# Kernel optimization log

Measured on AMD Instinct MI355X. Metric: run time of the kernel, lower is better.

## Reference

```python
import jax, jax.numpy as jnp
import numpy as np

B, TXT_T, MEL_T, N_MEL = 32, 256, 1600, 40
PAD_MAG = 1.0e12


def setup_inputs() -> dict:
    key = jax.random.key(0)
    k1, k2, k3, k4 = jax.random.split(key, 4)
    mu_logvar = jax.random.normal(k1, (B, TXT_T, 2 * N_MEL), jnp.float32)
    z = jax.random.normal(k2, (B, N_MEL, MEL_T), jnp.float32)
    text_lengths = jax.random.randint(k3, (B,), TXT_T // 2, TXT_T + 1).astype(jnp.int32)
    mel_lengths = jax.random.randint(k4, (B,), MEL_T // 2, MEL_T + 1).astype(jnp.int32)
    return {"mu_logvar": mu_logvar, "z": z,
            "text_lengths": text_lengths, "mel_lengths": mel_lengths}


def _mdn_log_prob(mu_logvar, z):
    # mu_logvar: [B, L, 2C], z: [B, C, T] -> log_prob_matrix [B, L, T]
    C = z.shape[1]
    mu, logvar = jnp.split(mu_logvar, 2, axis=-1)          # [B, L, C] each
    invvar = jnp.exp(-logvar)                               # [B, L, C]
    # mean_c((z - mu)^2 * invvar) expanded via matmuls (no [B,L,T,C] tensor)
    t1 = jnp.einsum('bct,blc->blt', z * z, invvar)
    t2 = jnp.einsum('bct,blc->blt', z, mu * invvar)
    t3 = jnp.sum(mu * mu * invvar, axis=-1)[:, :, None]
    mse = t1 - 2.0 * t2 + t3                                # [B, L, T]
    return -0.5 * (mse / C + jnp.mean(logvar, axis=-1)[:, :, None])


def _forward_dp(lp):
    # forward algorithm: log_alpha over (txt position, mel time) via scan over T
    Bb, L, T = lp.shape
    alpha0 = jnp.full((Bb, L + 1), -PAD_MAG, lp.dtype).at[:, 1].set(lp[:, 0, 0])

    def step(alpha, lp_t):
        stay = alpha[:, 1:] + 1e-7
        go = alpha[:, :-1] + 1e-7
        new = jnp.logaddexp(stay, go) + lp_t                # [B, L]
        alpha_new = jnp.concatenate(
            [jnp.full((Bb, 1), -PAD_MAG, lp.dtype), new], axis=1)
        return alpha_new, new

    _, ys = jax.lax.scan(step, alpha0, jnp.moveaxis(lp[:, :, 1:], 2, 0))
    log_alpha = jnp.concatenate([alpha0[:, 1:][None], ys], axis=0)  # [T, B, L]
    return log_alpha


def _viterbi(lp, text_lengths, mel_lengths):
    Bb, L, T = lp.shape
    beta0 = jnp.full((Bb, L), -PAD_MAG, lp.dtype).at[:, 0].set(lp[:, 0, 0])

    def fstep(beta, lp_t):
        shifted = jnp.concatenate(
            [jnp.full((Bb, 1), -PAD_MAG, lp.dtype), beta[:, :-1]], axis=1)
        new = jnp.maximum(beta, shifted) + lp_t
        return new, new

    _, ys = jax.lax.scan(fstep, beta0, jnp.moveaxis(lp[:, :, 1:], 2, 0))
    log_beta = jnp.transpose(jnp.concatenate([beta0[None], ys], axis=0), (1, 2, 0))  # [B, L, T]

    b_idx = jnp.arange(Bb)
    r0 = (text_lengths - 1).astype(jnp.float32)
    c0 = (mel_lengths - 1).astype(jnp.float32)

    def bstep(carry, _):
        rows, cols = carry
        ri = rows.astype(jnp.int32)
        ci = cols.astype(jnp.int32)
        # torch negative indexing wraps -> emulate with mod
        val_go = log_beta[b_idx, (ri - 1) % L, (ci - 1) % T]
        val_stay = log_beta[b_idx, ri % L, (ci - 1) % T]
        is_go = (val_go > val_stay).astype(rows.dtype)
        new_rows = jax.nn.relu(rows - is_go + 1.0) - 1.0
        new_cols = jax.nn.relu(cols) - 1.0
        return (new_rows, new_cols), new_rows

    _, path_ys = jax.lax.scan(bstep, (r0, c0), None, length=T - 1)
    full = jnp.concatenate([r0[None], path_ys], axis=0)     # [T, B], backward order
    path = full[::-1].T                                     # [B, T], chronological
    align = jax.nn.one_hot(path.astype(jnp.int32), L, dtype=lp.dtype)  # [B, T, L]

    def shift(a, ml):
        # F.pad(..., (-pad, pad)) on time axis: shift valid region to the front
        rolled = jnp.roll(a, -(T - ml), axis=0)
        mask = (jnp.arange(T) < ml)[:, None].astype(a.dtype)
        return rolled * mask

    return jax.vmap(shift)(align, mel_lengths)              # [B, T, L]


def reference(mu_logvar, z, text_lengths, mel_lengths):
    lp = _mdn_log_prob(mu_logvar, z)                        # [B, L, T]
    log_alpha = _forward_dp(lp)                             # [T, B, L]
    b_idx = jnp.arange(lp.shape[0])
    alpha_last = log_alpha[mel_lengths - 1, b_idx, text_lengths - 1]
    mdn_loss = -(alpha_last / mel_lengths.astype(alpha_last.dtype))  # [B]
    alignment = _viterbi(lp, text_lengths, mel_lengths)     # [B, T, L]
    return mdn_loss, alignment, lp
```

## Files before the change

### kernel.cpp

```cpp
#include <hip/hip_runtime.h>
#include <cstdint>
#include <math.h>

#define BB   32
#define LLEN 256
#define TLEN 1600
#define NC   40
#define NEGPADF (-1.0e12f)
#define NEGPADD (-1.0e12)
#define NBATCH 8
#define NPROD  4
#define NBUF   2

#define OFF_ALIGN 32
#define OFF_LP    (32 + (size_t)BB * TLEN * LLEN)

#define WSB_A    0
#define WSB_KC   (WSB_A + (size_t)BB * LLEN * 80 * 8)
#define WSB_LPT  (WSB_KC + (size_t)BB * LLEN * 8)
#define WSB_PATH (WSB_LPT + (size_t)BB * TLEN * LLEN * 4)

__device__ __forceinline__ int imin(int a, int b) { return a < b ? a : b; }

#define WAIT_LGKM0 0xC07F

__device__ __forceinline__ void bar_prod() {
  asm volatile("" ::: "memory");
  __builtin_amdgcn_s_waitcnt(WAIT_LGKM0);
  __builtin_amdgcn_s_barrier();
  asm volatile("" ::: "memory");
}
__device__ __forceinline__ void bar_cons() {
  asm volatile("" ::: "memory");
  __builtin_amdgcn_s_barrier();
  asm volatile("" ::: "memory");
}

__device__ __forceinline__ int rot1_i32(int x) {
  return __builtin_amdgcn_mov_dpp(x, 0x13C , 0xF, 0xF, true);
}
__device__ __forceinline__ float rot1_f32(float x) {
  return __int_as_float(rot1_i32(__float_as_int(x)));
}
__device__ __forceinline__ double rot1_f64(double x) {
  long long v = __double_as_longlong(x);
  int lo = rot1_i32((int)(v & 0xffffffffLL));
  int hi = rot1_i32((int)(v >> 32));
  return __longlong_as_double(((long long)hi << 32) | (unsigned long long)(unsigned int)lo);
}

__global__ __launch_bounds__(256) void prep_kernel(
    const float* __restrict__ mu_logvar, double* __restrict__ A, double* __restrict__ Kc) {
  int row = blockIdx.x * 4 + (threadIdx.x >> 6);
  int lane = threadIdx.x & 63;
  const float* src = mu_logvar + (size_t)row * (2 * NC);
  double mu = 0.0, lv = 0.0, iv = 0.0, part = 0.0;
  if (lane < NC) {
    mu = (double)src[lane];
    lv = (double)src[NC + lane];
    iv = exp(-lv);
    part = mu * mu * iv + lv;
  }
  for (int m = 1; m < 64; m <<= 1) part += __shfl_xor(part, m, 64);
  const double s = -0.5 / (double)NC;
  if (lane < NC) {
    A[(size_t)row * 80 + lane]      = s * iv;
    A[(size_t)row * 80 + NC + lane] = (1.0 / (double)NC) * mu * iv;
  }
  if (lane == 0) Kc[row] = s * part;
}

__global__ __launch_bounds__(128) void lp_kernel(
    const float* __restrict__ z, const double* __restrict__ A,
    const double* __restrict__ Kc, float* __restrict__ out,
    float* __restrict__ lpTh) {
  int b  = blockIdx.z;
  int l0 = blockIdx.y * 32;
  int t0 = blockIdx.x * 128;
  int tid = threadIdx.x;
  int t = t0 + tid;
  int tv = imin(t, TLEN - 1);
  bool act = (t < TLEN);

  float* lp_out = out + OFF_LP;
  float* loS    = out + OFF_ALIGN;

  float zr[NC];
  const float* zb = z + (size_t)b * NC * TLEN;
  #pragma unroll
  for (int c = 0; c < NC; ++c) zr[c] = zb[(size_t)c * TLEN + tv];

  __shared__ __align__(16) double tile[128][17];
  const double* Ab = A + ((size_t)b * LLEN + l0) * 80;
  const double* Kb = Kc + (size_t)b * LLEN + l0;

  for (int g = 0; g < 2; ++g) {
    for (int j16 = 0; j16 < 16; ++j16) {
      int j = g * 16 + j16;
      const double* Ar = Ab + (size_t)j * 80;
      double a0 = Kb[j], a1 = 0.0, a2 = 0.0, a3 = 0.0;
      #pragma unroll
      for (int c = 0; c < NC; c += 2) {
        double z0 = (double)zr[c], z1 = (double)zr[c + 1];
        a0 = fma(Ar[c],          z0 * z0, a0);
        a1 = fma(Ar[NC + c],     z0,      a1);
        a2 = fma(Ar[c + 1],      z1 * z1, a2);
        a3 = fma(Ar[NC + c + 1], z1,      a3);
      }
      double accd = (a0 + a2) + (a1 + a3);
      if (act) lp_out[((size_t)b * LLEN + l0 + j) * TLEN + t] = (float)accd;
      tile[tid][j16] = accd;
    }
    __syncthreads();
    #pragma unroll
    for (int p = 0; p < 4; ++p) {
      int idx = p * 128 + tid;
      int r = idx >> 2, c4 = idx & 3;
      int tr = t0 + r;
      if (tr < TLEN) {
        float h[4], lo[4];
        #pragma unroll
        for (int i = 0; i < 4; ++i) {
          double d = tile[r][c4 * 4 + i];
          float hh = (float)d;
          h[i] = hh;
          lo[i] = (float)(d - (double)hh);
        }
        size_t base = ((size_t)b * TLEN + tr) * LLEN + l0 + g * 16 + c4 * 4;
        *(float4*)(lpTh + base) = make_float4(h[0], h[1], h[2], h[3]);
        *(float4*)(loS + base)  = make_float4(lo[0], lo[1], lo[2], lo[3]);
      }
    }
    __syncthreads();
  }
}

__global__ __launch_bounds__(320, 1) void dp_kernel(
    const float* __restrict__ lpTh, const float* outR,
    const int* __restrict__ tlen, const int* __restrict__ mlen,
    float* __restrict__ out, int* __restrict__ pathg) {
  int bid = blockIdx.x;
  bool is_beta = (bid >= BB);
  int b = is_beta ? bid - BB : bid;
  int tid = threadIdx.x;
  int lane = tid & 63;
  int wv = tid >> 6;
  int tl = tlen[b];
  int ml = mlen[b];
  const float* lpb = lpTh + (size_t)b * TLEN * LLEN;
  const float* lob = outR + OFF_ALIGN + (size_t)b * TLEN * LLEN;
  int nint = (ml - 2 + NBATCH) / NBATCH;

  __shared__ double   bufd[NBUF][NBATCH][4][64];
  __shared__ float    bufa[NBUF][NBATCH][4][64];
  __shared__ uint32_t Dbits[LLEN][TLEN / 32];

  if (wv >= 1) {
    int q = wv - 1;
    const float* ph = lpb + 4 * lane;
    const float* pl = lob + 4 * lane;
    float4 vh[NBATCH], vl[NBATCH];
    auto issue = [&](int w) {
      #pragma unroll
      for (int j = 0; j < NBATCH; ++j) {
        int c = imin(1 + NBATCH * w + j, TLEN - 1);
        vh[j] = *(const float4*)(ph + (size_t)c * LLEN);
        if (is_beta) vl[j] = *(const float4*)(pl + (size_t)c * LLEN);
      }
    };
    auto store = [&](int w) {
      int s = w % NBUF;
      if (is_beta) {
        #pragma unroll
        for (int j = 0; j < NBATCH; ++j) {
          bufd[s][j][0][lane] = (double)vh[j].x + (double)vl[j].x;
          bufd[s][j][1][lane] = (double)vh[j].y + (double)vl[j].y;
          bufd[s][j][2][lane] = (double)vh[j].z + (double)vl[j].z;
          bufd[s][j][3][lane] = (double)vh[j].w + (double)vl[j].w;
        }
      } else {
        #pragma unroll
        for (int j = 0; j < NBATCH; ++j) {
          bufa[s][j][0][lane] = vh[j].x;
          bufa[s][j][1][lane] = vh[j].y;
          bufa[s][j][2][lane] = vh[j].z;
          bufa[s][j][3][lane] = vh[j].w;
        }
      }
    };
    if (q < nint) issue(q);
    if (q == 0) {
      store(0);
      if (NPROD < nint) issue(NPROD);
    }
    for (int w = 0; w < nint; ++w) {
      bar_prod();
      int nw = w + 1;
      if (nw < nint && (nw % NPROD) == q) {
        store(nw);
        int fw = nw + NPROD;
        if (fw < nint) issue(fw);
      }
    }
  } else if (!is_beta) {
    float lp00 = lpb[0];
    float o0 = (lane == 0) ? lp00 : NEGPADF;
    float o1 = NEGPADF, o2 = NEGPADF, o3 = NEGPADF;
    float f0 = o0, f1 = o1, f2 = o2, f3 = o3;
    float q = rot1_f32(o3);
    int t = 1;
    for (int w = 0; w < nint; ++w) {
      bar_cons();
      int s = w % NBUF;
      #pragma unroll
      for (int j = 0; j < NBATCH; ++j, ++t) {
        float l0 = bufa[s][j][0][lane];
        float l1 = bufa[s][j][1][lane];
        float l2 = bufa[s][j][2][lane];
        float l3 = bufa[s][j][3][lane];
        float p = (lane == 0) ? NEGPADF : q;
        float m0 = fmaxf(o0, p),  d0 = fabsf(o0 - p);
        float m1 = fmaxf(o1, o0), d1 = fabsf(o1 - o0);
        float m2 = fmaxf(o2, o1), d2 = fabsf(o2 - o1);
        float m3 = fmaxf(o3, o2), d3 = fabsf(o3 - o2);
        float n0 = m0 + 1e-7f + __logf(1.0f + __expf(-d0)) + l0;
        float n1 = m1 + 1e-7f + __logf(1.0f + __expf(-d1)) + l1;
        float n2 = m2 + 1e-7f + __logf(1.0f + __expf(-d2)) + l2;
        float n3 = m3 + 1e-7f + __logf(1.0f + __expf(-d3)) + l3;
        o0 = n0; o1 = n1; o2 = n2; o3 = n3;
        q = rot1_f32(o3);
        if (t == ml - 1) { f0 = o0; f1 = o1; f2 = o2; f3 = o3; }
      }
    }
    int fr = tl - 1;
    if (lane == (fr >> 2)) {
      int sx = fr & 3;
      float val = (sx == 0) ? f0 : (sx == 1) ? f1 : (sx == 2) ? f2 : f3;
      out[b] = -val / (float)ml;
    }
  } else {
    double lp00 = (double)lpb[0] + (double)lob[0];
    double o0 = (lane == 0) ? lp00 : NEGPADD;
    double o1 = NEGPADD, o2 = NEGPADD, o3 = NEGPADD;
    uint32_t a0 = 0, a1 = (lane == 0) ? 1u : 0u, a2 = 0, a3 = 0;
    double q = rot1_f64(o3);
    int t = 1;
    for (int w = 0; w < nint; ++w) {
      bar_cons();
      int s = w % NBUF;
      #pragma unroll
      for (int j = 0; j < NBATCH; ++j, ++t) {
        double l0 = bufd[s][j][0][lane];
        double l1 = bufd[s][j][1][lane];
        double l2 = bufd[s][j][2][lane];
        double l3 = bufd[s][j][3][lane];
        double p = (lane == 0) ? NEGPADD : q;
        double n0 = fmax(o0, p)  + l0;
        double n1 = fmax(o1, o0) + l1;
        double n2 = fmax(o2, o1) + l2;
        double n3 = fmax(o3, o2) + l3;
        q = rot1_f64(n3);
        uint32_t bit = 1u << (t & 31);
        if (q  > n0) a0 |= bit;
        if (n0 > n1) a1 |= bit;
        if (n1 > n2) a2 |= bit;
        if (n2 > n3) a3 |= bit;
        o0 = n0; o1 = n1; o2 = n2; o3 = n3;
        if ((t & 31) == 31) {
          int wd = t >> 5;
          Dbits[4 * lane + 0][wd] = a0; a0 = 0;
          Dbits[4 * lane + 1][wd] = a1; a1 = 0;
          Dbits[4 * lane + 2][wd] = a2; a2 = 0;
          Dbits[4 * lane + 3][wd] = a3; a3 = 0;
        }
      }
    }
    int tend = nint * NBATCH;
    int wd = tend >> 5;
    if ((tend & 31) != 31 && wd < TLEN / 32) {
      Dbits[4 * lane + 0][wd] = a0;
      Dbits[4 * lane + 1][wd] = a1;
      Dbits[4 * lane + 2][wd] = a2;
      Dbits[4 * lane + 3][wd] = a3;
    }
    __builtin_amdgcn_s_waitcnt(WAIT_LGKM0);

    if (lane == 0) {
      int* pb = pathg + b * TLEN;
      int r = tl - 1;
      pb[ml - 1] = r;
      int curR = 1 << 30, curW = -1;
      uint32_t W = 0;
      for (int qq = ml - 2; qq >= 0; --qq) {
        int w2 = qq >> 5;
        if (r >= 0 && (r != curR || w2 != curW)) { W = Dbits[r][w2]; curR = r; curW = w2; }
        int g = (r >= 0) ? (int)((W >> (qq & 31)) & 1u) : 0;
        r -= g;
        pb[qq] = r;
      }
    }
  }
}

__global__ __launch_bounds__(256) void finalize_kernel(
    const int* __restrict__ mlen, const int* __restrict__ pathg,
    float* __restrict__ out) {
  int b = blockIdx.y;
  int t0 = blockIdx.x * 8;
  float* al = out + OFF_ALIGN + (size_t)b * TLEN * LLEN;
  float4 z4 = make_float4(0.f, 0.f, 0.f, 0.f);
  #pragma unroll
  for (int p = 0; p < 2; ++p) {
    int idx = p * 256 + threadIdx.x;
    int r = idx >> 6, c4 = idx & 63;
    *(float4*)(al + (size_t)(t0 + r) * LLEN + c4 * 4) = z4;
  }
  __syncthreads();
  if (threadIdx.x < 8) {
    int t = t0 + threadIdx.x;
    int ml = mlen[b];
    if (t < ml) {
      int p = pathg[b * TLEN + t];
      if (p >= 0) al[(size_t)t * LLEN + p] = 1.0f;
    }
  }
}

extern "C" void kernel_launch(void* const* d_in, const int* in_sizes, int n_in,
                              void* d_out, int out_size, void* d_ws, size_t ws_size,
                              hipStream_t stream) {
  const float* mu_logvar = (const float*)d_in[0];
  const float* z         = (const float*)d_in[1];
  const int*   tlv       = (const int*)d_in[2];
  const int*   mlv       = (const int*)d_in[3];
  float* out = (float*)d_out;
  char*  wsb = (char*)d_ws;

  double* Ad   = (double*)(wsb + WSB_A);
  double* Kcd  = (double*)(wsb + WSB_KC);
  float*  lpTh = (float*)(wsb + WSB_LPT);
  int*    path = (int*)(wsb + WSB_PATH);

  prep_kernel<<<dim3(BB * LLEN / 4), 256, 0, stream>>>(mu_logvar, Ad, Kcd);
  lp_kernel<<<dim3(13, 8, BB), 128, 0, stream>>>(z, Ad, Kcd, out, lpTh);
  dp_kernel<<<dim3(2 * BB), 320, 0, stream>>>(lpTh, out, tlv, mlv, out, path);
  finalize_kernel<<<dim3(TLEN / 8, BB), 256, 0, stream>>>(mlv, path, out);
}
```

Baseline: 560.1 us.

## Fuse alignment finalize into DP kernel and use base-2 log-add-exp

Removes the separate finalize kernel: producer waves of the Viterbi blocks zero the alignment rows once their data is consumed, and the backtracked path is kept in LDS and scattered by the same block. The forward recurrence is rescaled to base 2 so it can use native exp2/log2 intrinsics, with the epsilon pre-folded into the staged inputs. The batch per barrier is doubled, with loads split into two sub-batches, to reduce barrier count. This risks write/read ordering issues on the shared alignment buffer and adds store traffic into the serial DP kernel.

```diff
diff --git a/kernel.cpp b/kernel.cpp
--- a/kernel.cpp
+++ b/kernel.cpp
@@ -8,9 +8,14 @@
 #define NC   40
 #define NEGPADF (-1.0e12f)
 #define NEGPADD (-1.0e12)
-#define NBATCH 8
+#define NBATCH 16
+#define SUBB   8
 #define NPROD  4
 #define NBUF   2
+
+#define LOG2E_F 1.4426950408889634f
+#define LN2_F   0.6931471805599453f
+#define C7F     1.4426950408889634e-7f
 
 #define OFF_ALIGN 32
 #define OFF_LP    (32 + (size_t)BB * TLEN * LLEN)
@@ -18,7 +23,6 @@
 #define WSB_A    0
 #define WSB_KC   (WSB_A + (size_t)BB * LLEN * 80 * 8)
 #define WSB_LPT  (WSB_KC + (size_t)BB * LLEN * 8)
-#define WSB_PATH (WSB_LPT + (size_t)BB * TLEN * LLEN * 4)
 
 __device__ __forceinline__ int imin(int a, int b) { return a < b ? a : b; }
 
@@ -138,7 +142,7 @@
 __global__ __launch_bounds__(320, 1) void dp_kernel(
     const float* __restrict__ lpTh, const float* outR,
     const int* __restrict__ tlen, const int* __restrict__ mlen,
-    float* __restrict__ out, int* __restrict__ pathg) {
+    float* __restrict__ out) {
   int bid = blockIdx.x;
   bool is_beta = (bid >= BB);
   int b = is_beta ? bid - BB : bid;
@@ -149,86 +153,104 @@
   int ml = mlen[b];
   const float* lpb = lpTh + (size_t)b * TLEN * LLEN;
   const float* lob = outR + OFF_ALIGN + (size_t)b * TLEN * LLEN;
+  float* al = out + OFF_ALIGN + (size_t)b * TLEN * LLEN;
   int nint = (ml - 2 + NBATCH) / NBATCH;
 
-  __shared__ double   bufd[NBUF][NBATCH][4][64];
-  __shared__ float    bufa[NBUF][NBATCH][4][64];
+  __shared__ __align__(16) double bufd[NBUF][NBATCH][4][64];
   __shared__ uint32_t Dbits[LLEN][TLEN / 32];
+  __shared__ int pathL[TLEN];
+  float* bufaF = (float*)&bufd[0][0][0][0];
 
   if (wv >= 1) {
     int q = wv - 1;
+    int nsb = 2 * nint;
     const float* ph = lpb + 4 * lane;
     const float* pl = lob + 4 * lane;
-    float4 vh[NBATCH], vl[NBATCH];
-    auto issue = [&](int w) {
+    float4 vh[SUBB], vl[SUBB];
+    float4 z4 = make_float4(0.f, 0.f, 0.f, 0.f);
+    auto issue = [&](int sb) {
       #pragma unroll
-      for (int j = 0; j < NBATCH; ++j) {
-        int c = imin(1 + NBATCH * w + j, TLEN - 1);
+      for (int j = 0; j < SUBB; ++j) {
+        int c = imin(1 + SUBB * sb + j, TLEN - 1);
         vh[j] = *(const float4*)(ph + (size_t)c * LLEN);
         if (is_beta) vl[j] = *(const float4*)(pl + (size_t)c * LLEN);
       }
     };
-    auto store = [&](int w) {
-      int s = w % NBUF;
+    auto store = [&](int sb) {
+      int s  = (sb >> 1) % NBUF;
+      int jb = (sb & 1) * SUBB;
       if (is_beta) {
         #pragma unroll
-        for (int j = 0; j < NBATCH; ++j) {
-          bufd[s][j][0][lane] = (double)vh[j].x + (double)vl[j].x;
-          bufd[s][j][1][lane] = (double)vh[j].y + (double)vl[j].y;
-          bufd[s][j][2][lane] = (double)vh[j].z + (double)vl[j].z;
-          bufd[s][j][3][lane] = (double)vh[j].w + (double)vl[j].w;
+        for (int j = 0; j < SUBB; ++j) {
+          bufd[s][jb + j][0][lane] = (double)vh[j].x + (double)vl[j].x;
+          bufd[s][jb + j][1][lane] = (double)vh[j].y + (double)vl[j].y;
+          bufd[s][jb + j][2][lane] = (double)vh[j].z + (double)vl[j].z;
+          bufd[s][jb + j][3][lane] = (double)vh[j].w + (double)vl[j].w;
         }
       } else {
         #pragma unroll
-        for (int j = 0; j < NBATCH; ++j) {
-          bufa[s][j][0][lane] = vh[j].x;
-          bufa[s][j][1][lane] = vh[j].y;
-          bufa[s][j][2][lane] = vh[j].z;
-          bufa[s][j][3][lane] = vh[j].w;
+        for (int j = 0; j < SUBB; ++j) {
+          int off = ((s * NBATCH + jb + j) * 4) * 64 + lane;
+          bufaF[off]       = fmaf(vh[j].x, LOG2E_F, C7F);
+          bufaF[off + 64]  = fmaf(vh[j].y, LOG2E_F, C7F);
+          bufaF[off + 128] = fmaf(vh[j].z, LOG2E_F, C7F);
+          bufaF[off + 192] = fmaf(vh[j].w, LOG2E_F, C7F);
         }
       }
     };
-    if (q < nint) issue(q);
-    if (q == 0) {
-      store(0);
-      if (NPROD < nint) issue(NPROD);
+    if (q < 2) {
+      issue(q); store(q);
+      if (q + NPROD < nsb) issue(q + NPROD);
+    } else if (q < nsb) {
+      issue(q);
     }
     for (int w = 0; w < nint; ++w) {
       bar_prod();
-      int nw = w + 1;
-      if (nw < nint && (nw % NPROD) == q) {
-        store(nw);
-        int fw = nw + NPROD;
-        if (fw < nint) issue(fw);
-      }
+      int sb0 = 2 * w + 2;
+      int mine = ((sb0 & 3) == q) ? sb0 : ((((sb0 + 1) & 3) == q) ? (sb0 + 1) : -1);
+      if (mine >= 0 && mine < nsb) {
+        store(mine);
+        if (mine + NPROD < nsb) issue(mine + NPROD);
+      }
+      if (is_beta && w >= 1) {
+        int zc = NBATCH * (w - 1) + 4 * q;
+        float* az = al + (size_t)zc * LLEN + 4 * lane;
+        #pragma unroll
+        for (int k = 0; k < 4; ++k) *(float4*)(az + (size_t)k * LLEN) = z4;
+      }
+    }
+    if (is_beta) {
+      for (int c = NBATCH * (nint - 1) + q; c < TLEN; c += NPROD)
+        *(float4*)(al + (size_t)c * LLEN + 4 * lane) = z4;
     }
   } else if (!is_beta) {
-    float lp00 = lpb[0];
+    float lp00 = lpb[0] * LOG2E_F;
     float o0 = (lane == 0) ? lp00 : NEGPADF;
     float o1 = NEGPADF, o2 = NEGPADF, o3 = NEGPADF;
     float f0 = o0, f1 = o1, f2 = o2, f3 = o3;
-    float q = rot1_f32(o3);
+    float qv = rot1_f32(o3);
     int t = 1;
     for (int w = 0; w < nint; ++w) {
       bar_cons();
       int s = w % NBUF;
       #pragma unroll
       for (int j = 0; j < NBATCH; ++j, ++t) {
-        float l0 = bufa[s][j][0][lane];
-        float l1 = bufa[s][j][1][lane];
-        float l2 = bufa[s][j][2][lane];
-        float l3 = bufa[s][j][3][lane];
-        float p = (lane == 0) ? NEGPADF : q;
-        float m0 = fmaxf(o0, p),  d0 = fabsf(o0 - p);
-        float m1 = fmaxf(o1, o0), d1 = fabsf(o1 - o0);
-        float m2 = fmaxf(o2, o1), d2 = fabsf(o2 - o1);
-        float m3 = fmaxf(o3, o2), d3 = fabsf(o3 - o2);
-        float n0 = m0 + 1e-7f + __logf(1.0f + __expf(-d0)) + l0;
-        float n1 = m1 + 1e-7f + __logf(1.0f + __expf(-d1)) + l1;
-        float n2 = m2 + 1e-7f + __logf(1.0f + __expf(-d2)) + l2;
-        float n3 = m3 + 1e-7f + __logf(1.0f + __expf(-d3)) + l3;
+        int off = ((s * NBATCH + j) * 4) * 64 + lane;
+        float l0 = bufaF[off];
+        float l1 = bufaF[off + 64];
+        float l2 = bufaF[off + 128];
+        float l3 = bufaF[off + 192];
+        float p = (lane == 0) ? NEGPADF : qv;
+        float m0 = fmaxf(o0, p),  d0 = o0 - p;
+        float m1 = fmaxf(o1, o0), d1 = o1 - o0;
+        float m2 = fmaxf(o2, o1), d2 = o2 - o1;
+        float m3 = fmaxf(o3, o2), d3 = o3 - o2;
+        float n0 = m0 + __builtin_amdgcn_logf(1.0f + __builtin_amdgcn_exp2f(-fabsf(d0))) + l0;
+        float n1 = m1 + __builtin_amdgcn_logf(1.0f + __builtin_amdgcn_exp2f(-fabsf(d1))) + l1;
+        float n2 = m2 + __builtin_amdgcn_logf(1.0f + __builtin_amdgcn_exp2f(-fabsf(d2))) + l2;
+        float n3 = m3 + __builtin_amdgcn_logf(1.0f + __builtin_amdgcn_exp2f(-fabsf(d3))) + l3;
         o0 = n0; o1 = n1; o2 = n2; o3 = n3;
-        q = rot1_f32(o3);
+        qv = rot1_f32(o3);
         if (t == ml - 1) { f0 = o0; f1 = o1; f2 = o2; f3 = o3; }
       }
     }
@@ -236,14 +258,14 @@
     if (lane == (fr >> 2)) {
       int sx = fr & 3;
       float val = (sx == 0) ? f0 : (sx == 1) ? f1 : (sx == 2) ? f2 : f3;
-      out[b] = -val / (float)ml;
+      out[b] = -val * LN2_F / (float)ml;
     }
   } else {
     double lp00 = (double)lpb[0] + (double)lob[0];
     double o0 = (lane == 0) ? lp00 : NEGPADD;
     double o1 = NEGPADD, o2 = NEGPADD, o3 = NEGPADD;
     uint32_t a0 = 0, a1 = (lane == 0) ? 1u : 0u, a2 = 0, a3 = 0;
-    double q = rot1_f64(o3);
+    double qv = rot1_f64(o3);
     int t = 1;
     for (int w = 0; w < nint; ++w) {
       bar_cons();
@@ -254,14 +276,14 @@
         double l1 = bufd[s][j][1][lane];
         double l2 = bufd[s][j][2][lane];
         double l3 = bufd[s][j][3][lane];
-        double p = (lane == 0) ? NEGPADD : q;
+        double p = (lane == 0) ? NEGPADD : qv;
         double n0 = fmax(o0, p)  + l0;
         double n1 = fmax(o1, o0) + l1;
         double n2 = fmax(o2, o1) + l2;
         double n3 = fmax(o3, o2) + l3;
-        q = rot1_f64(n3);
+        qv = rot1_f64(n3);
         uint32_t bit = 1u << (t & 31);
-        if (q  > n0) a0 |= bit;
+        if (qv > n0) a0 |= bit;
         if (n0 > n1) a1 |= bit;
         if (n1 > n2) a2 |= bit;
         if (n2 > n3) a3 |= bit;
@@ -286,9 +308,8 @@
     __builtin_amdgcn_s_waitcnt(WAIT_LGKM0);
 
     if (lane == 0) {
-      int* pb = pathg + b * TLEN;
       int r = tl - 1;
-      pb[ml - 1] = r;
+      pathL[ml - 1] = r;
       int curR = 1 << 30, curW = -1;
       uint32_t W = 0;
       for (int qq = ml - 2; qq >= 0; --qq) {
@@ -296,31 +317,15 @@
         if (r >= 0 && (r != curR || w2 != curW)) { W = Dbits[r][w2]; curR = r; curW = w2; }
         int g = (r >= 0) ? (int)((W >> (qq & 31)) & 1u) : 0;
         r -= g;
-        pb[qq] = r;
-      }
-    }
-  }
-}
-
-__global__ __launch_bounds__(256) void finalize_kernel(
-    const int* __restrict__ mlen, const int* __restrict__ pathg,
-    float* __restrict__ out) {
-  int b = blockIdx.y;
-  int t0 = blockIdx.x * 8;
-  float* al = out + OFF_ALIGN + (size_t)b * TLEN * LLEN;
-  float4 z4 = make_float4(0.f, 0.f, 0.f, 0.f);
-  #pragma unroll
-  for (int p = 0; p < 2; ++p) {
-    int idx = p * 256 + threadIdx.x;
-    int r = idx >> 6, c4 = idx & 63;
-    *(float4*)(al + (size_t)(t0 + r) * LLEN + c4 * 4) = z4;
-  }
-  __syncthreads();
-  if (threadIdx.x < 8) {
-    int t = t0 + threadIdx.x;
-    int ml = mlen[b];
-    if (t < ml) {
-      int p = pathg[b * TLEN + t];
+        pathL[qq] = r;
+      }
+    }
+  }
+
+  if (is_beta) {
+    __syncthreads();
+    for (int t = tid; t < ml; t += 320) {
+      int p = pathL[t];
       if (p >= 0) al[(size_t)t * LLEN + p] = 1.0f;
     }
   }
@@ -339,10 +344,8 @@
   double* Ad   = (double*)(wsb + WSB_A);
   double* Kcd  = (double*)(wsb + WSB_KC);
   float*  lpTh = (float*)(wsb + WSB_LPT);
-  int*    path = (int*)(wsb + WSB_PATH);
 
   prep_kernel<<<dim3(BB * LLEN / 4), 256, 0, stream>>>(mu_logvar, Ad, Kcd);
   lp_kernel<<<dim3(13, 8, BB), 128, 0, stream>>>(z, Ad, Kcd, out, lpTh);
-  dp_kernel<<<dim3(2 * BB), 320, 0, stream>>>(lpTh, out, tlv, mlv, out, path);
-  finalize_kernel<<<dim3(TLEN / 8, BB), 256, 0, stream>>>(mlv, path, out);
-}
+  dp_kernel<<<dim3(2 * BB), 320, 0, stream>>>(lpTh, out, tlv, mlv, out);
+}
```

Measured after the change: 516.0 us. 7.9% less time.
